# Optimization experiments

Hardware: AMD Instinct MI355X
Metric: run time of the kernel (lower is better)

## Reference

```python
import jax, jax.numpy as jnp
import numpy as np

B, N, C = 64, 197, 768
H = 12
D = C // H
SCALE = D ** -0.5
TAU = 5.0
THRESHOLD = 0.6
NEG_INF = float('-inf')


def setup_inputs() -> dict:
    key = jax.random.key(0)
    ks = jax.random.split(key, 10)
    def gumbel(k, shape):
        # -log(Exponential) == standard Gumbel noise, matches torch exponential_().log()
        e = jax.random.exponential(k, shape, dtype=jnp.float32)
        return -jnp.log(e + 1e-10)
    s = 0.02
    return {
        'x': jax.random.normal(ks[0], (B, N, C), dtype=jnp.float32),
        'g1': gumbel(ks[1], (B, N - 1, 1)),
        'g2': gumbel(ks[2], (B, N - 1, 1)),
        'Wq': jax.random.normal(ks[3], (C, C), dtype=jnp.float32) * s,
        'Wk': jax.random.normal(ks[4], (C, C), dtype=jnp.float32) * s,
        'Wv': jax.random.normal(ks[5], (C, C), dtype=jnp.float32) * s,
        'Wp': jax.random.normal(ks[6], (C, C), dtype=jnp.float32) * s,
        'bp': jnp.zeros((C,), dtype=jnp.float32),
        'Wm': jax.random.normal(ks[7], (1, C), dtype=jnp.float32) * s,
        'bm': jnp.zeros((1,), dtype=jnp.float32),
    }


def reference(x, g1, g2, Wq, Wk, Wv, Wp, bp, Wm, bm):
    b, n, c = x.shape
    # QKV projections (qkv_bias=False), reshape to (B, H, N, D)
    q = (x @ Wq.T).reshape(b, n, H, D).transpose(0, 2, 1, 3)
    k = (x @ Wk.T).reshape(b, n, H, D).transpose(0, 2, 1, 3)
    v = (x @ Wv.T).reshape(b, n, H, D).transpose(0, 2, 1, 3)

    attn_pre = jnp.einsum('bhnd,bhmd->bhnm', q, k) * SCALE  # (B,H,N,N)

    # SimpleTokenSelect: gumbel-sigmoid gating on non-CLS tokens (training=True, hard=True)
    logits = x[:, 1:] @ Wm.T + bm                       # (B, N-1, 1)
    y_soft = jax.nn.sigmoid((logits + g1 - g2) / TAU)
    y_hard = (y_soft > THRESHOLD).astype(y_soft.dtype)
    ts = y_hard - jax.lax.stop_gradient(y_soft) + y_soft  # straight-through
    ts = jnp.concatenate([jnp.ones((b, 1, 1), dtype=ts.dtype), ts], axis=1)[..., 0]  # (B, N)

    # attention policy = outer product of token gates, detached (ada_token_detach_attn)
    policy = jax.lax.stop_gradient(jnp.einsum('bn,bm->bnm', ts, ts))[:, None]  # (B,1,N,N)

    # pre-softmax masking: zero gated scores, -inf off-diagonal entries of gated rows
    eye = jnp.eye(n, dtype=attn_pre.dtype)
    neg_mask = jnp.where(1.0 - policy - eye > 0, NEG_INF, 0.0)
    attn = jax.nn.softmax(attn_pre * policy + neg_mask, axis=-1)

    out = jnp.einsum('bhnm,bhmd->bhnd', attn, v)        # (B,H,N,D)
    out = out.transpose(0, 2, 1, 3).reshape(b, n, c)
    out = out @ Wp.T + bp                                # proj (dropout p=0)
    return out
```

## Files before the change

kernel.cpp:

```cpp
#include <hip/hip_runtime.h>
#include <hip/hip_bf16.h>
#include <cstdint>

typedef unsigned short u16;
typedef __attribute__((ext_vector_type(8))) short bf16x8;
typedef __attribute__((ext_vector_type(4))) float f32x4;

#define NB 64
#define NN 197
#define NC 768
#define NH 12
#define ND 64
#define NM (NB*NN)
#define CAP 96
#define NT 24
#define ASZ ((size_t)NM*NC)
#define WSZ ((size_t)NC*NC)
#define SELSZ ((size_t)NB*CAP*NC)

#define WAITVM(N) asm volatile("s_waitcnt vmcnt(" #N ")" ::: "memory")
#define SBAR() __builtin_amdgcn_s_barrier()
#define SCHEDB() __builtin_amdgcn_sched_barrier(0)

__device__ __forceinline__ u16 f2bf(float f) {
  uint32_t u = __float_as_uint(f);
  u += 0x7fffu + ((u >> 16) & 1u);
  return (u16)(u >> 16);
}

__device__ __forceinline__ void gl_lds16(const u16* g, u16* l) {
  __builtin_amdgcn_global_load_lds(
      (const __attribute__((address_space(1))) void*)g,
      (__attribute__((address_space(3))) void*)l, 16, 0, 0);
}

__device__ __forceinline__ int self_compact(const float* __restrict__ ts, int b,
                                            int* sidx, unsigned long long* bmask) {
  int t = threadIdx.x, lane = t & 63, wave = t >> 6;
  bool sel = (t < NN) && (ts[b * NN + t] > 0.5f);
  unsigned long long m = __ballot(sel);
  if (lane == 0) bmask[wave] = m;
  for (int i = t; i < CAP; i += 256) sidx[i] = 0;
  __syncthreads();
  int before = 0, total = 0;
  #pragma unroll
  for (int w = 0; w < 4; ++w) {
    int c = __popcll(bmask[w]);
    total += c;
    if (w < wave) before += c;
  }
  int within = __popcll(bmask[wave] & ((lane == 0) ? 0ull : (~0ull >> (64 - lane))));
  int pos = before + within;
  int cntc = total < CAP ? total : CAP;
  if (sel && pos < CAP) sidx[pos] = t;
  __syncthreads();
  return cntc;
}

#define GATEB 3152
#define WBLK 576
#define TRBLK 144
__global__ __launch_bounds__(256) void k1_prep(const float* __restrict__ x,
    const float* __restrict__ g1, const float* __restrict__ g2,
    const float* __restrict__ Wm, const float* __restrict__ bm,
    const float* __restrict__ wq, const float* __restrict__ wk,
    const float* __restrict__ wv, const float* __restrict__ wp,
    u16* __restrict__ xb, u16* __restrict__ wqb, u16* __restrict__ wkb,
    u16* __restrict__ wvb, u16* __restrict__ wpb, u16* __restrict__ wvt,
    float* __restrict__ ts) {
  __shared__ u16 T[64][72];
  int bid = blockIdx.x, tid = threadIdx.x;

  if (bid < GATEB) {
    int wave = tid >> 6, lane = tid & 63;
    int wid = bid * 4 + wave;
    int b = wid / NN, n = wid % NN;
    const float* xr = x + (size_t)wid * NC;
    u16* xbr = xb + (size_t)wid * NC;
    double acc = 0.0;
    #pragma unroll
    for (int i = 0; i < 3; ++i) {
      float4 f = *(const float4*)(xr + lane * 4 + 256 * i);
      float4 w = *(const float4*)(Wm + lane * 4 + 256 * i);
      acc += (double)f.x * w.x + (double)f.y * w.y
           + (double)f.z * w.z + (double)f.w * w.w;
      ushort4 o;
      o.x = f2bf(f.x); o.y = f2bf(f.y); o.z = f2bf(f.z); o.w = f2bf(f.w);
      *(ushort4*)(xbr + lane * 4 + 256 * i) = o;
    }
    #pragma unroll
    for (int off = 32; off; off >>= 1) acc += __shfl_down(acc, off);
    float o = 1.0f;
    if (n != 0) {
      double z = (acc + (double)bm[0] + (double)g1[b*(NN-1) + n - 1]
                                      - (double)g2[b*(NN-1) + n - 1]) / 5.0;
      o = (z > 0.4054651081081643820) ? 1.0f : 0.0f;
    }
    if (lane == 0) ts[wid] = o;
    return;
  }
  bid -= GATEB;
  if (bid < 4*WBLK) {
    int seg = bid / WBLK;
    int i = (bid - seg * WBLK) * 256 + tid;
    const float* src; u16* dst;
    if (seg == 0)      { src = wq; dst = wqb; }
    else if (seg == 1) { src = wk; dst = wkb; }
    else if (seg == 2) { src = wv; dst = wvb; }
    else               { src = wp; dst = wpb; }
    float4 f = ((const float4*)src)[i];
    ushort4 o;
    o.x = f2bf(f.x); o.y = f2bf(f.y); o.z = f2bf(f.z); o.w = f2bf(f.w);
    ((ushort4*)dst)[i] = o;
    return;
  }
  bid -= 4*WBLK;
  {
    int bx = bid % 12, by = bid / 12;
    int j0 = by * 64, k0 = bx * 64;
    #pragma unroll
    for (int g = 0; g < 4; ++g) {
      int r = g * 16 + (tid >> 4);
      int c4 = (tid & 15) * 4;
      float4 f = *(const float4*)(wv + (size_t)(j0 + r) * NC + k0 + c4);
      T[c4 + 0][r] = f2bf(f.x);
      T[c4 + 1][r] = f2bf(f.y);
      T[c4 + 2][r] = f2bf(f.z);
      T[c4 + 3][r] = f2bf(f.w);
    }
    __syncthreads();
    #pragma unroll
    for (int g = 0; g < 4; ++g) {
      int r = g * 16 + (tid >> 4);
      int c4 = (tid & 15) * 4;
      ushort4 o = *(ushort4*)&T[r][c4];
      *(ushort4*)(wvt + (size_t)(k0 + r) * NC + j0 + c4) = o;
    }
  }
}

__global__ __launch_bounds__(256) void k2_wvp_qkv(const u16* __restrict__ xb,
    const u16* __restrict__ wq3, const u16* __restrict__ wpb,
    const u16* __restrict__ wvt, u16* __restrict__ wvpb,
    u16* __restrict__ sel3, const float* __restrict__ ts) {
  alignas(16) __shared__ u16 SA[3][128][32];
  alignas(16) __shared__ u16 SB[3][128][32];
  __shared__ int sidx[CAP];
  __shared__ unsigned long long bmask[4];
  int bid = blockIdx.x;
  int tid = threadIdx.x, lane = tid & 63, wave = tid >> 6;
  int lr = lane & 15, lg = lane >> 4, lk = lg * 8;

  if (bid < 36) {
    int m0 = (bid / 6) * 128, n0 = (bid % 6) * 128;
    int wr = (wave >> 1) * 64, wc = (wave & 1) * 64;
    f32x4 acc[4][4];
    #pragma unroll
    for (int i = 0; i < 4; ++i)
      #pragma unroll
      for (int j = 0; j < 4; ++j) acc[i][j] = (f32x4){0.f,0.f,0.f,0.f};
    auto stage = [&](int buf, int kt) {
      int k0 = kt * 32;
      #pragma unroll
      for (int i = 0; i < 2; ++i) {
        int c = wave * 2 + i;
        int id = c * 64 + lane;
        int row = id >> 2, col8 = (id & 3) * 8;
        gl_lds16(wpb + (size_t)(m0 + row) * NC + k0 + col8, &SA[buf][0][0] + c * 512);
        gl_lds16(wvt + (size_t)(n0 + row) * NC + k0 + col8, &SB[buf][0][0] + c * 512);
      }
    };
    auto comp = [&](int buf) {
      bf16x8 af[4], bfr[4];
      #pragma unroll
      for (int f = 0; f < 4; ++f) {
        af[f]  = *(const bf16x8*)(&SA[buf][wr + f*16 + lr][lk]);
        bfr[f] = *(const bf16x8*)(&SB[buf][wc + f*16 + lr][lk]);
      }
      #pragma unroll
      for (int i = 0; i < 4; ++i)
        #pragma unroll
        for (int j = 0; j < 4; ++j)
          acc[i][j] = __builtin_amdgcn_mfma_f32_16x16x32_bf16(af[i], bfr[j], acc[i][j], 0, 0, 0);
    };
    stage(0, 0); stage(1, 1);
    int cb = 0;
    for (int t = 0; t < NT; ++t) {
      if (t + 2 < NT) {
        int sb = cb + 2; if (sb > 2) sb -= 3;
        stage(sb, t + 2);
        WAITVM(8);
      } else if (t + 1 < NT) { WAITVM(4); }
      else { WAITVM(0); }
      SBAR(); SCHEDB();
      comp(cb);
      SBAR();
      cb = (cb == 2) ? 0 : cb + 1;
    }
    #pragma unroll
    for (int i = 0; i < 4; ++i)
      #pragma unroll
      for (int j = 0; j < 4; ++j)
        #pragma unroll
        for (int r = 0; r < 4; ++r)
          wvpb[(size_t)(m0 + wr + i*16 + 4*lg + r) * NC + n0 + wc + j*16 + lr] =
              f2bf(acc[i][j][r]);
    return;
  }

  int t0 = bid - 36;
  int gb = t0 / 18, r18 = t0 % 18;
  int y = r18 / 3, z = r18 % 3;
  int b = gb / 3, rc = gb % 3;
  int cntb = self_compact(ts, b, sidx, bmask);
  if (rc * 32 >= cntb) return;
  const u16* W = wq3 + (size_t)z * WSZ;
  u16* o = sel3 + (size_t)z * SELSZ;
  int n0 = y * 128;

  int chA = wave * 64 + lane;
  int tokA = sidx[rc * 32 + (chA >> 2)];
  const u16* baseA = xb + (size_t)(b * NN + tokA) * NC + (chA & 3) * 8;
  int chB0 = wave * 64 + lane, chB1 = 256 + wave * 64 + lane;
  const u16* baseB0 = W + (size_t)(n0 + (chB0 >> 2)) * NC + (chB0 & 3) * 8;
  const u16* baseB1 = W + (size_t)(n0 + (chB1 >> 2)) * NC + (chB1 & 3) * 8;

  int wc = wave * 32;
  bool hasA = (wave < 2);
  f32x4 acc[2][2];
  #pragma unroll
  for (int i = 0; i < 2; ++i)
    #pragma unroll
    for (int j = 0; j < 2; ++j) acc[i][j] = (f32x4){0.f,0.f,0.f,0.f};

  auto stageS = [&](int buf, int kt) {
    int k0 = kt * 32;
    if (hasA) gl_lds16(baseA + k0, &SA[buf][0][0] + (size_t)(wave * 64) * 8);
    gl_lds16(baseB0 + k0, &SB[buf][0][0] + (size_t)(wave * 64) * 8);
    gl_lds16(baseB1 + k0, &SB[buf][0][0] + (size_t)(256 + wave * 64) * 8);
  };
  auto compS = [&](int buf) {
    bf16x8 af[2], bfr[2];
    #pragma unroll
    for (int f = 0; f < 2; ++f) {
      af[f]  = *(const bf16x8*)(&SA[buf][f*16 + lr][lk]);
      bfr[f] = *(const bf16x8*)(&SB[buf][wc + f*16 + lr][lk]);
    }
    #pragma unroll
    for (int i = 0; i < 2; ++i)
      #pragma unroll
      for (int j = 0; j < 2; ++j)
        acc[i][j] = __builtin_amdgcn_mfma_f32_16x16x32_bf16(af[i], bfr[j], acc[i][j], 0, 0, 0);
  };
  stageS(0, 0); stageS(1, 1);
  int cb = 0;
  for (int tt = 0; tt < NT; ++tt) {
    if (tt + 2 < NT) {
      int sb = cb + 2; if (sb > 2) sb -= 3;
      stageS(sb, tt + 2);
      if (hasA) { WAITVM(6); } else { WAITVM(4); }
    } else if (tt + 1 < NT) {
      if (hasA) { WAITVM(3); } else { WAITVM(2); }
    } else { WAITVM(0); }
    SBAR(); SCHEDB();
    compS(cb);
    SBAR();
    cb = (cb == 2) ? 0 : cb + 1;
  }

  #pragma unroll
  for (int i = 0; i < 2; ++i)
    #pragma unroll
    for (int j = 0; j < 2; ++j)
      #pragma unroll
      for (int r = 0; r < 4; ++r) {
        int rsel = rc*32 + i*16 + 4*lg + r;
        if (rsel < cntb)
          o[(size_t)(b * CAP + rsel) * NC + n0 + wc + j*16 + lr] = f2bf(acc[i][j][r]);
      }
}

__global__ __launch_bounds__(256) void attn_sel(const u16* __restrict__ qsel,
    const u16* __restrict__ ksel, const u16* __restrict__ vsel,
    u16* __restrict__ zsel, const float* __restrict__ ts) {
  alignas(16) __shared__ u16 Vt[64][232];
  __shared__ unsigned long long bmask[4];
  int bh = blockIdx.x;
  int b = bh / NH, h = bh % NH;
  int tid = threadIdx.x, lane = tid & 63, wave = tid >> 6;
  int lr = lane & 15, lg = lane >> 4;
  const size_t qbase = (size_t)b * CAP * NC + (size_t)h * ND;

  bool selt = (tid < NN) && (ts[b * NN + tid] > 0.5f);
  unsigned long long m = __ballot(selt);
  if (lane == 0) bmask[wave] = m;
  __syncthreads();
  int cntb = 0;
  #pragma unroll
  for (int w = 0; w < 4; ++w) cntb += __popcll(bmask[w]);
  if (cntb > CAP) cntb = CAP;

  for (int id = tid; id < cntb * 8; id += 256) {
    int i = id >> 3, c8 = (id & 7) * 8;
    int4 val = *(const int4*)(vsel + qbase + (size_t)i * NC + c8);
    u16 tmp[8];
    *(int4*)tmp = val;
    #pragma unroll
    for (int e = 0; e < 8; ++e) Vt[c8 + e][i] = tmp[e];
  }
  for (int id = tid; id < 64 * 32; id += 256)
    Vt[id >> 5][cntb + (id & 31)] = 0;
  __syncthreads();

  int nchunk = (cntb + 15) >> 4;
  int mtmax  = nchunk;
  int mcmax  = (cntb + 31) >> 5;
  int idx0 = (((lane & 15) | ((lane & 16) << 1))) << 2;
  int idx1 = idx0 + 64;

  for (int qc = wave; qc < nchunk; qc += 4) {
    const u16* qp = qsel + qbase + (size_t)(qc * 16 + lr) * NC + lg * 8;
    bf16x8 qf0 = *(const bf16x8*)(qp);
    bf16x8 qf1 = *(const bf16x8*)(qp + 32);

    f32x4 s[6];
    #pragma unroll
    for (int mt = 0; mt < 6; ++mt) s[mt] = (f32x4){0.f,0.f,0.f,0.f};
    #pragma unroll
    for (int mt = 0; mt < 6; ++mt) {
      if (mt < mtmax) {
        const u16* kp = ksel + qbase + (size_t)(mt * 16 + lr) * NC + lg * 8;
        bf16x8 kf0 = *(const bf16x8*)(kp);
        bf16x8 kf1 = *(const bf16x8*)(kp + 32);
        f32x4 a = (f32x4){0.f,0.f,0.f,0.f};
        a = __builtin_amdgcn_mfma_f32_16x16x32_bf16(kf0, qf0, a, 0, 0, 0);
        a = __builtin_amdgcn_mfma_f32_16x16x32_bf16(kf1, qf1, a, 0, 0, 0);
        s[mt] = a;
      }
    }

    float mx = -3e38f;
    #pragma unroll
    for (int mt = 0; mt < 6; ++mt)
      #pragma unroll
      for (int jj = 0; jj < 4; ++jj) {
        int mm = mt*16 + 4*lg + jj;
        float val = (mm < cntb) ? s[mt][jj] * 0.125f : -1e30f;
        s[mt][jj] = val;
        mx = fmaxf(mx, val);
      }
    mx = fmaxf(mx, __shfl_xor(mx, 16));
    mx = fmaxf(mx, __shfl_xor(mx, 32));
    float sum = 0.f;
    #pragma unroll
    for (int mt = 0; mt < 6; ++mt)
      #pragma unroll
      for (int jj = 0; jj < 4; ++jj) {
        float pv = __expf(s[mt][jj] - mx);
        s[mt][jj] = pv;
        sum += pv;
      }
    sum += __shfl_xor(sum, 16);
    sum += __shfl_xor(sum, 32);
    float inv = 1.0f / sum;

    uint32_t u[6][2];
    #pragma unroll
    for (int mt = 0; mt < 6; ++mt) {
      u[mt][0] = ((uint32_t)f2bf(s[mt][1]*inv) << 16) | f2bf(s[mt][0]*inv);
      u[mt][1] = ((uint32_t)f2bf(s[mt][3]*inv) << 16) | f2bf(s[mt][2]*inv);
    }

    f32x4 oacc[4];
    #pragma unroll
    for (int dt = 0; dt < 4; ++dt) oacc[dt] = (f32x4){0.f,0.f,0.f,0.f};
    #pragma unroll
    for (int mc = 0; mc < 3; ++mc) {
      if (mc < mcmax) {
        uint32_t a0 = (uint32_t)__builtin_amdgcn_ds_bpermute(idx0, (int)u[2*mc][0]);
        uint32_t b0 = (uint32_t)__builtin_amdgcn_ds_bpermute(idx0, (int)u[2*mc+1][0]);
        uint32_t a1 = (uint32_t)__builtin_amdgcn_ds_bpermute(idx0, (int)u[2*mc][1]);
        uint32_t b1 = (uint32_t)__builtin_amdgcn_ds_bpermute(idx0, (int)u[2*mc+1][1]);
        uint32_t a2 = (uint32_t)__builtin_amdgcn_ds_bpermute(idx1, (int)u[2*mc][0]);
        uint32_t b2 = (uint32_t)__builtin_amdgcn_ds_bpermute(idx1, (int)u[2*mc+1][0]);
        uint32_t a3 = (uint32_t)__builtin_amdgcn_ds_bpermute(idx1, (int)u[2*mc][1]);
        uint32_t b3 = (uint32_t)__builtin_amdgcn_ds_bpermute(idx1, (int)u[2*mc+1][1]);
        bool hi = (lg >= 2);
        union { uint32_t w[4]; bf16x8 v; } pu;
        pu.w[0] = hi ? b0 : a0;
        pu.w[1] = hi ? b1 : a1;
        pu.w[2] = hi ? b2 : a2;
        pu.w[3] = hi ? b3 : a3;
        bf16x8 pa = pu.v;
        #pragma unroll
        for (int dt = 0; dt < 4; ++dt) {
          bf16x8 vf = *(const bf16x8*)(&Vt[dt*16 + lr][mc*32 + lg*8]);
          oacc[dt] = __builtin_amdgcn_mfma_f32_16x16x32_bf16(pa, vf, oacc[dt], 0, 0, 0);
        }
      }
    }

    #pragma unroll
    for (int r = 0; r < 4; ++r) {
      int nloc = qc*16 + 4*lg + r;
      if (nloc < cntb) {
        u16* op = zsel + qbase + (size_t)nloc * NC + lr;
        #pragma unroll
        for (int dt = 0; dt < 4; ++dt)
          op[dt*16] = f2bf(oacc[dt][r]);
      }
    }
  }
}

#define DBLK 594
#define PBLK 1152
__global__ __launch_bounds__(256) void k4_out(const u16* __restrict__ xb,
    const u16* __restrict__ wvpb, const u16* __restrict__ zsel,
    const u16* __restrict__ wpb, const float* __restrict__ ts,
    const float* __restrict__ bp, float* __restrict__ out) {
  alignas(16) __shared__ u16 SA[3][128][32];
  alignas(16) __shared__ u16 SB[3][128][32];
  __shared__ int sidx[CAP];
  __shared__ unsigned long long bmask[4];
  int bid = blockIdx.x;
  int tid = threadIdx.x, lane = tid & 63, wave = tid >> 6;
  int lr = lane & 15, lg = lane >> 4, lk = lg * 8;

  if (bid < DBLK) {
    int orig = bid;
    int xcd = orig & 7, loc = orig >> 3;
    int wgid = (xcd < 2 ? xcd * 75 : 150 + (xcd - 2) * 74) + loc;
    int m0 = (wgid / 6) * 128, n0 = (wgid % 6) * 128;
    int wr = (wave >> 1) * 64, wc = (wave & 1) * 64;
    f32x4 acc[4][4];
    #pragma unroll
    for (int i = 0; i < 4; ++i)
      #pragma unroll
      for (int j = 0; j < 4; ++j) acc[i][j] = (f32x4){0.f,0.f,0.f,0.f};
    auto stage = [&](int buf, int kt) {
      int k0 = kt * 32;
      #pragma unroll
      for (int i = 0; i < 2; ++i) {
        int c = wave * 2 + i;
        int id = c * 64 + lane;
        int row = id >> 2, col8 = (id & 3) * 8;
        gl_lds16(xb + (size_t)(m0 + row) * NC + k0 + col8, &SA[buf][0][0] + c * 512);
        gl_lds16(wvpb + (size_t)(n0 + row) * NC + k0 + col8, &SB[buf][0][0] + c * 512);
      }
    };
    auto comp = [&](int buf) {
      bf16x8 af[4], bfr[4];
      #pragma unroll
      for (int f = 0; f < 4; ++f) {
        af[f]  = *(const bf16x8*)(&SA[buf][wr + f*16 + lr][lk]);
        bfr[f] = *(const bf16x8*)(&SB[buf][wc + f*16 + lr][lk]);
      }
      #pragma unroll
      for (int i = 0; i < 4; ++i)
        #pragma unroll
        for (int j = 0; j < 4; ++j)
          acc[i][j] = __builtin_amdgcn_mfma_f32_16x16x32_bf16(af[i], bfr[j], acc[i][j], 0, 0, 0);
    };
    stage(0, 0); stage(1, 1);
    int cb = 0;
    for (int t = 0; t < NT; ++t) {
      if (t + 2 < NT) {
        int sb = cb + 2; if (sb > 2) sb -= 3;
        stage(sb, t + 2);
        WAITVM(8);
      } else if (t + 1 < NT) { WAITVM(4); }
      else { WAITVM(0); }
      SBAR(); SCHEDB();
      comp(cb);
      SBAR();
      cb = (cb == 2) ? 0 : cb + 1;
    }
    #pragma unroll
    for (int i = 0; i < 4; ++i) {
      int rbase = m0 + wr + i*16 + 4*lg;
      #pragma unroll
      for (int j = 0; j < 4; ++j) {
        int col = n0 + wc + j*16 + lr;
        #pragma unroll
        for (int r = 0; r < 4; ++r) {
          int row = rbase + r;
          if (row < NM && ts[row] < 0.5f)
            out[(size_t)row * NC + col] = acc[i][j][r] + bp[col];
        }
      }
    }
    return;
  }

  int t = bid - DBLK;
  int gb = t / 6, y = t % 6;
  int b = gb / 3, rc = gb % 3;
  int cntb = self_compact(ts, b, sidx, bmask);
  if (rc * 32 >= cntb) return;
  int n0 = y * 128;

  int chA = wave * 64 + lane;
  const u16* baseA = zsel + (size_t)(b * CAP + rc * 32 + (chA >> 2)) * NC + (chA & 3) * 8;
  int chB0 = wave * 64 + lane, chB1 = 256 + wave * 64 + lane;
  const u16* baseB0 = wpb + (size_t)(n0 + (chB0 >> 2)) * NC + (chB0 & 3) * 8;
  const u16* baseB1 = wpb + (size_t)(n0 + (chB1 >> 2)) * NC + (chB1 & 3) * 8;

  int wc = wave * 32;
  f32x4 acc[2][2];
  #pragma unroll
  for (int i = 0; i < 2; ++i)
    #pragma unroll
    for (int j = 0; j < 2; ++j) acc[i][j] = (f32x4){0.f,0.f,0.f,0.f};

  auto stageS = [&](int buf, int k0) {
    if (wave < 2) gl_lds16(baseA + k0, &SA[buf][0][0] + (size_t)(wave * 64) * 8);
    gl_lds16(baseB0 + k0, &SB[buf][0][0] + (size_t)(wave * 64) * 8);
    gl_lds16(baseB1 + k0, &SB[buf][0][0] + (size_t)(256 + wave * 64) * 8);
  };
  auto compS = [&](int buf) {
    bf16x8 af[2], bfr[2];
    #pragma unroll
    for (int f = 0; f < 2; ++f) {
      af[f]  = *(const bf16x8*)(&SA[buf][f*16 + lr][lk]);
      bfr[f] = *(const bf16x8*)(&SB[buf][wc + f*16 + lr][lk]);
    }
    #pragma unroll
    for (int i = 0; i < 2; ++i)
      #pragma unroll
      for (int j = 0; j < 2; ++j)
        acc[i][j] = __builtin_amdgcn_mfma_f32_16x16x32_bf16(af[i], bfr[j], acc[i][j], 0, 0, 0);
  };
  stageS(0, 0);
  __syncthreads();
  int cur = 0;
  for (int tt = 0; tt < NT - 1; ++tt) {
    stageS(cur ^ 1, (tt + 1) * 32);
    compS(cur);
    __syncthreads();
    cur ^= 1;
  }
  compS(cur);

  #pragma unroll
  for (int i = 0; i < 2; ++i)
    #pragma unroll
    for (int j = 0; j < 2; ++j)
      #pragma unroll
      for (int r = 0; r < 4; ++r) {
        int rsel = rc*32 + i*16 + 4*lg + r;
        if (rsel < cntb) {
          int tok = sidx[rsel];
          int col = n0 + wc + j*16 + lr;
          out[(size_t)(b * NN + tok) * NC + col] = acc[i][j][r] + bp[col];
        }
      }
}

extern "C" void kernel_launch(void* const* d_in, const int* in_sizes, int n_in,
                              void* d_out, int out_size, void* d_ws, size_t ws_size,
                              hipStream_t stream) {
  const float* x  = (const float*)d_in[0];
  const float* g1 = (const float*)d_in[1];
  const float* g2 = (const float*)d_in[2];
  const float* Wq = (const float*)d_in[3];
  const float* Wk = (const float*)d_in[4];
  const float* Wv = (const float*)d_in[5];
  const float* Wp = (const float*)d_in[6];
  const float* bp = (const float*)d_in[7];
  const float* Wm = (const float*)d_in[8];
  const float* bm = (const float*)d_in[9];
  float* out = (float*)d_out;

  const size_t act_sz = ASZ * 2;
  const size_t w_sz   = WSZ * 2;
  const size_t sel_sz = SELSZ * 2;
  size_t need = act_sz + 4*sel_sz + 6*w_sz + (size_t)NM*4 + 256;
  if (ws_size < need) return;

  char* p = (char*)d_ws;
  u16* xb   = (u16*)p; p += act_sz;
  u16* qsel = (u16*)p; p += sel_sz;
  u16* ksel = (u16*)p; p += sel_sz;
  u16* vsel = (u16*)p; p += sel_sz;
  u16* zsel = (u16*)p; p += sel_sz;
  u16* wqb  = (u16*)p; p += w_sz;
  u16* wkb  = (u16*)p; p += w_sz;
  u16* wvb  = (u16*)p; p += w_sz;
  u16* wpb  = (u16*)p; p += w_sz;
  u16* wvtb = (u16*)p; p += w_sz;
  u16* wvpb = (u16*)p; p += w_sz;
  float* ts = (float*)p;
  (void)wkb; (void)wvb;

  k1_prep<<<dim3(GATEB + 4*WBLK + TRBLK), 256, 0, stream>>>(
      x, g1, g2, Wm, bm, Wq, Wk, Wv, Wp,
      xb, wqb, wkb, wvb, wpb, wvtb, ts);

  k2_wvp_qkv<<<dim3(36 + NB*3*18), 256, 0, stream>>>(
      xb, wqb, wpb, wvtb, wvpb, qsel, ts);

  attn_sel<<<dim3(NB*NH), 256, 0, stream>>>(qsel, ksel, vsel, zsel, ts);

  k4_out<<<dim3(DBLK + PBLK), 256, 0, stream>>>(
      xb, wvpb, zsel, wpb, ts, bp, out);
}
```

Baseline: 108.1 us.

## Shrink dense out-GEMM tile to 128x64, single-buffer LDS, share union LDS

Halves the N-tile of the dense V·Wp GEMM path from 128 to 64 columns, doubling its block count and remapping the XCD-aware block-to-tile assignment. The triple-buffered async pipeline is replaced with a simple single-buffer load/sync/compute/sync loop. LDS is merged into one union buffer shared by the dense and the sparse path. The aim is lower per-block LDS and register use, giving more blocks for occupancy and load balance, at the cost of losing load/compute overlap and re-reading A tiles twice.

```diff
diff --git a/kernel.cpp b/kernel.cpp
--- a/kernel.cpp
+++ b/kernel.cpp
@@ -413,14 +413,13 @@
   }
 }
 
-#define DBLK 594
+#define DBLK 1188
 #define PBLK 1152
 __global__ __launch_bounds__(256) void k4_out(const u16* __restrict__ xb,
     const u16* __restrict__ wvpb, const u16* __restrict__ zsel,
     const u16* __restrict__ wpb, const float* __restrict__ ts,
     const float* __restrict__ bp, float* __restrict__ out) {
-  alignas(16) __shared__ u16 SA[3][128][32];
-  alignas(16) __shared__ u16 SB[3][128][32];
+  alignas(16) __shared__ u16 LDSU[10496];
   __shared__ int sidx[CAP];
   __shared__ unsigned long long bmask[4];
   int bid = blockIdx.x;
@@ -428,59 +427,50 @@
   int lr = lane & 15, lg = lane >> 4, lk = lg * 8;
 
   if (bid < DBLK) {
-    int orig = bid;
-    int xcd = orig & 7, loc = orig >> 3;
-    int wgid = (xcd < 2 ? xcd * 75 : 150 + (xcd - 2) * 74) + loc;
-    int m0 = (wgid / 6) * 128, n0 = (wgid % 6) * 128;
-    int wr = (wave >> 1) * 64, wc = (wave & 1) * 64;
-    f32x4 acc[4][4];
+    u16 (*As)[32] = reinterpret_cast<u16(*)[32]>(&LDSU[0]);
+    u16 (*Bs)[32] = reinterpret_cast<u16(*)[32]>(&LDSU[4096]);
+    int xcd = bid & 7, loc = bid >> 3;
+    int wgid = (xcd < 4 ? xcd * 149 : 596 + (xcd - 4) * 148) + loc;
+    int m0 = (wgid / 12) * 128, n0 = (wgid % 12) * 64;
+    int wr = (wave >> 1) * 64, wc = (wave & 1) * 32;
+    int idA0 = wave * 64 + lane;
+    int idA1 = (4 + wave) * 64 + lane;
+    int idB  = wave * 64 + lane;
+    const u16* srcA0 = xb + (size_t)(m0 + (idA0 >> 2)) * NC + (idA0 & 3) * 8;
+    const u16* srcA1 = xb + (size_t)(m0 + (idA1 >> 2)) * NC + (idA1 & 3) * 8;
+    const u16* srcB  = wvpb + (size_t)(n0 + (idB >> 2)) * NC + (idB & 3) * 8;
+    u16* dA0 = &As[0][0] + (size_t)wave * 512;
+    u16* dA1 = &As[0][0] + (size_t)(4 + wave) * 512;
+    u16* dB  = &Bs[0][0] + (size_t)wave * 512;
+
+    f32x4 acc[4][2];
     #pragma unroll
     for (int i = 0; i < 4; ++i)
       #pragma unroll
-      for (int j = 0; j < 4; ++j) acc[i][j] = (f32x4){0.f,0.f,0.f,0.f};
-    auto stage = [&](int buf, int kt) {
-      int k0 = kt * 32;
-      #pragma unroll
-      for (int i = 0; i < 2; ++i) {
-        int c = wave * 2 + i;
-        int id = c * 64 + lane;
-        int row = id >> 2, col8 = (id & 3) * 8;
-        gl_lds16(xb + (size_t)(m0 + row) * NC + k0 + col8, &SA[buf][0][0] + c * 512);
-        gl_lds16(wvpb + (size_t)(n0 + row) * NC + k0 + col8, &SB[buf][0][0] + c * 512);
-      }
-    };
-    auto comp = [&](int buf) {
-      bf16x8 af[4], bfr[4];
-      #pragma unroll
-      for (int f = 0; f < 4; ++f) {
-        af[f]  = *(const bf16x8*)(&SA[buf][wr + f*16 + lr][lk]);
-        bfr[f] = *(const bf16x8*)(&SB[buf][wc + f*16 + lr][lk]);
-      }
+      for (int j = 0; j < 2; ++j) acc[i][j] = (f32x4){0.f,0.f,0.f,0.f};
+
+    for (int k0 = 0; k0 < NC; k0 += 32) {
+      gl_lds16(srcA0 + k0, dA0);
+      gl_lds16(srcA1 + k0, dA1);
+      gl_lds16(srcB + k0, dB);
+      __syncthreads();
+      bf16x8 af[4], bfr[2];
+      #pragma unroll
+      for (int f = 0; f < 4; ++f) af[f] = *(const bf16x8*)(&As[wr + f*16 + lr][lk]);
+      #pragma unroll
+      for (int f = 0; f < 2; ++f) bfr[f] = *(const bf16x8*)(&Bs[wc + f*16 + lr][lk]);
       #pragma unroll
       for (int i = 0; i < 4; ++i)
         #pragma unroll
-        for (int j = 0; j < 4; ++j)
+        for (int j = 0; j < 2; ++j)
           acc[i][j] = __builtin_amdgcn_mfma_f32_16x16x32_bf16(af[i], bfr[j], acc[i][j], 0, 0, 0);
-    };
-    stage(0, 0); stage(1, 1);
-    int cb = 0;
-    for (int t = 0; t < NT; ++t) {
-      if (t + 2 < NT) {
-        int sb = cb + 2; if (sb > 2) sb -= 3;
-        stage(sb, t + 2);
-        WAITVM(8);
-      } else if (t + 1 < NT) { WAITVM(4); }
-      else { WAITVM(0); }
-      SBAR(); SCHEDB();
-      comp(cb);
-      SBAR();
-      cb = (cb == 2) ? 0 : cb + 1;
+      __syncthreads();
     }
     #pragma unroll
     for (int i = 0; i < 4; ++i) {
       int rbase = m0 + wr + i*16 + 4*lg;
       #pragma unroll
-      for (int j = 0; j < 4; ++j) {
+      for (int j = 0; j < 2; ++j) {
         int col = n0 + wc + j*16 + lr;
         #pragma unroll
         for (int r = 0; r < 4; ++r) {
@@ -493,6 +483,8 @@
     return;
   }
 
+  u16 (*PA)[32][32]  = reinterpret_cast<u16(*)[32][32]>(&LDSU[0]);
+  u16 (*PB)[128][32] = reinterpret_cast<u16(*)[128][32]>(&LDSU[2048]);
   int t = bid - DBLK;
   int gb = t / 6, y = t % 6;
   int b = gb / 3, rc = gb % 3;
@@ -514,16 +506,16 @@
     for (int j = 0; j < 2; ++j) acc[i][j] = (f32x4){0.f,0.f,0.f,0.f};
 
   auto stageS = [&](int buf, int k0) {
-    if (wave < 2) gl_lds16(baseA + k0, &SA[buf][0][0] + (size_t)(wave * 64) * 8);
-    gl_lds16(baseB0 + k0, &SB[buf][0][0] + (size_t)(wave * 64) * 8);
-    gl_lds16(baseB1 + k0, &SB[buf][0][0] + (size_t)(256 + wave * 64) * 8);
+    if (wave < 2) gl_lds16(baseA + k0, &PA[buf][0][0] + (size_t)(wave * 64) * 8);
+    gl_lds16(baseB0 + k0, &PB[buf][0][0] + (size_t)(wave * 64) * 8);
+    gl_lds16(baseB1 + k0, &PB[buf][0][0] + (size_t)(256 + wave * 64) * 8);
   };
   auto compS = [&](int buf) {
     bf16x8 af[2], bfr[2];
     #pragma unroll
     for (int f = 0; f < 2; ++f) {
-      af[f]  = *(const bf16x8*)(&SA[buf][f*16 + lr][lk]);
-      bfr[f] = *(const bf16x8*)(&SB[buf][wc + f*16 + lr][lk]);
+      af[f]  = *(const bf16x8*)(&PA[buf][f*16 + lr][lk]);
+      bfr[f] = *(const bf16x8*)(&PB[buf][wc + f*16 + lr][lk]);
     }
     #pragma unroll
     for (int i = 0; i < 2; ++i)
```

After: 108.4 us. About the same (+0.3%).

## Globally compact selected tokens into packed rows for full-size 128x128 GEMM tiles

Applied to the files above, without the earlier changes.

Adds a single-block compaction kernel that builds a global index of gated tokens across all batches with per-batch offsets. The selected-row QKV and output-projection GEMMs then run as dense 128x128 MFMA tiles over the packed rows, replacing per-batch 32-row tiles that wasted work and recomputed the compaction in every block. In exchange, the new selected and dense k4 GEMM loops lose the triple-buffered pipeline and become single-buffered with two barriers per k-step. The serial single-block compaction launch adds latency on the critical path.

```diff
diff --git a/kernel.cpp b/kernel.cpp
--- a/kernel.cpp
+++ b/kernel.cpp
@@ -14,9 +14,11 @@
 #define NM (NB*NN)
 #define CAP 96
 #define NT 24
+#define SELR 6144
+#define MSELT 48
 #define ASZ ((size_t)NM*NC)
 #define WSZ ((size_t)NC*NC)
-#define SELSZ ((size_t)NB*CAP*NC)
+#define SELSZ2 ((size_t)SELR*NC)
 
 #define WAITVM(N) asm volatile("s_waitcnt vmcnt(" #N ")" ::: "memory")
 #define SBAR() __builtin_amdgcn_s_barrier()
@@ -32,29 +34,6 @@
   __builtin_amdgcn_global_load_lds(
       (const __attribute__((address_space(1))) void*)g,
       (__attribute__((address_space(3))) void*)l, 16, 0, 0);
-}
-
-__device__ __forceinline__ int self_compact(const float* __restrict__ ts, int b,
-                                            int* sidx, unsigned long long* bmask) {
-  int t = threadIdx.x, lane = t & 63, wave = t >> 6;
-  bool sel = (t < NN) && (ts[b * NN + t] > 0.5f);
-  unsigned long long m = __ballot(sel);
-  if (lane == 0) bmask[wave] = m;
-  for (int i = t; i < CAP; i += 256) sidx[i] = 0;
-  __syncthreads();
-  int before = 0, total = 0;
-  #pragma unroll
-  for (int w = 0; w < 4; ++w) {
-    int c = __popcll(bmask[w]);
-    total += c;
-    if (w < wave) before += c;
-  }
-  int within = __popcll(bmask[wave] & ((lane == 0) ? 0ull : (~0ull >> (64 - lane))));
-  int pos = before + within;
-  int cntc = total < CAP ? total : CAP;
-  if (sel && pos < CAP) sidx[pos] = t;
-  __syncthreads();
-  return cntc;
 }
 
 #define GATEB 3152
@@ -139,166 +118,181 @@
   }
 }
 
+__global__ __launch_bounds__(256) void ck_compact(const float* __restrict__ ts,
+    int* __restrict__ cnt, int* __restrict__ boff, int* __restrict__ gidx) {
+  __shared__ unsigned long long bm[4];
+  __shared__ int runoff;
+  int tid = threadIdx.x, lane = tid & 63, wave = tid >> 6;
+  if (tid == 0) runoff = 0;
+  __syncthreads();
+  for (int b = 0; b < NB; ++b) {
+    bool sel = (tid < NN) && (ts[b * NN + tid] > 0.5f);
+    unsigned long long m = __ballot(sel);
+    if (lane == 0) bm[wave] = m;
+    __syncthreads();
+    int before = 0, total = 0;
+    #pragma unroll
+    for (int w = 0; w < 4; ++w) {
+      int c = __popcll(bm[w]);
+      total += c;
+      if (w < wave) before += c;
+    }
+    int within = __popcll(bm[wave] & ((lane == 0) ? 0ull : (~0ull >> (64 - lane))));
+    int pos = before + within;
+    int cc = total < CAP ? total : CAP;
+    int base = runoff;
+    if (sel && pos < CAP) gidx[base + pos] = b * NN + tid;
+    __syncthreads();
+    if (tid == 0) { cnt[b] = cc; boff[b] = base; runoff = base + cc; }
+    __syncthreads();
+  }
+  int tot = runoff;
+  if (tid == 0) boff[NB] = tot;
+  for (int i = tot + tid; i < SELR; i += 256) gidx[i] = 0;
+}
+
 __global__ __launch_bounds__(256) void k2_wvp_qkv(const u16* __restrict__ xb,
     const u16* __restrict__ wq3, const u16* __restrict__ wpb,
     const u16* __restrict__ wvt, u16* __restrict__ wvpb,
-    u16* __restrict__ sel3, const float* __restrict__ ts) {
+    u16* __restrict__ sel3, const int* __restrict__ boff,
+    const int* __restrict__ gidx) {
   alignas(16) __shared__ u16 SA[3][128][32];
   alignas(16) __shared__ u16 SB[3][128][32];
-  __shared__ int sidx[CAP];
-  __shared__ unsigned long long bmask[4];
   int bid = blockIdx.x;
   int tid = threadIdx.x, lane = tid & 63, wave = tid >> 6;
   int lr = lane & 15, lg = lane >> 4, lk = lg * 8;
 
-  if (bid < 36) {
-    int m0 = (bid / 6) * 128, n0 = (bid % 6) * 128;
+  if (bid < MSELT * 18) {
+    int mt = bid / 18, r18 = bid % 18;
+    int z = r18 / 6, y = r18 % 6;
+    int total = boff[NB];
+    int m0 = mt * 128;
+    if (m0 >= total) return;
+    const u16* W = wq3 + (size_t)z * WSZ;
+    u16* o = sel3 + (size_t)z * SELSZ2;
+    int n0 = y * 128;
     int wr = (wave >> 1) * 64, wc = (wave & 1) * 64;
+
+    int id0 = (wave*2 + 0) * 64 + lane, id1 = (wave*2 + 1) * 64 + lane;
+    const u16* baseA0 = xb + (size_t)gidx[m0 + (id0 >> 2)] * NC + (id0 & 3) * 8;
+    const u16* baseA1 = xb + (size_t)gidx[m0 + (id1 >> 2)] * NC + (id1 & 3) * 8;
+    const u16* baseB0 = W + (size_t)(n0 + (id0 >> 2)) * NC + (id0 & 3) * 8;
+    const u16* baseB1 = W + (size_t)(n0 + (id1 >> 2)) * NC + (id1 & 3) * 8;
+    u16* dA0 = &SA[0][0][0] + (size_t)(wave*2 + 0) * 512;
+    u16* dA1 = &SA[0][0][0] + (size_t)(wave*2 + 1) * 512;
+    u16* dB0 = &SB[0][0][0] + (size_t)(wave*2 + 0) * 512;
+    u16* dB1 = &SB[0][0][0] + (size_t)(wave*2 + 1) * 512;
+
     f32x4 acc[4][4];
     #pragma unroll
     for (int i = 0; i < 4; ++i)
       #pragma unroll
       for (int j = 0; j < 4; ++j) acc[i][j] = (f32x4){0.f,0.f,0.f,0.f};
-    auto stage = [&](int buf, int kt) {
-      int k0 = kt * 32;
-      #pragma unroll
-      for (int i = 0; i < 2; ++i) {
-        int c = wave * 2 + i;
-        int id = c * 64 + lane;
-        int row = id >> 2, col8 = (id & 3) * 8;
-        gl_lds16(wpb + (size_t)(m0 + row) * NC + k0 + col8, &SA[buf][0][0] + c * 512);
-        gl_lds16(wvt + (size_t)(n0 + row) * NC + k0 + col8, &SB[buf][0][0] + c * 512);
-      }
-    };
-    auto comp = [&](int buf) {
+
+    for (int k0 = 0; k0 < NC; k0 += 32) {
+      gl_lds16(baseA0 + k0, dA0);
+      gl_lds16(baseA1 + k0, dA1);
+      gl_lds16(baseB0 + k0, dB0);
+      gl_lds16(baseB1 + k0, dB1);
+      __syncthreads();
       bf16x8 af[4], bfr[4];
       #pragma unroll
       for (int f = 0; f < 4; ++f) {
-        af[f]  = *(const bf16x8*)(&SA[buf][wr + f*16 + lr][lk]);
-        bfr[f] = *(const bf16x8*)(&SB[buf][wc + f*16 + lr][lk]);
+        af[f]  = *(const bf16x8*)(&SA[0][wr + f*16 + lr][lk]);
+        bfr[f] = *(const bf16x8*)(&SB[0][wc + f*16 + lr][lk]);
       }
       #pragma unroll
       for (int i = 0; i < 4; ++i)
         #pragma unroll
         for (int j = 0; j < 4; ++j)
           acc[i][j] = __builtin_amdgcn_mfma_f32_16x16x32_bf16(af[i], bfr[j], acc[i][j], 0, 0, 0);
-    };
-    stage(0, 0); stage(1, 1);
-    int cb = 0;
-    for (int t = 0; t < NT; ++t) {
-      if (t + 2 < NT) {
-        int sb = cb + 2; if (sb > 2) sb -= 3;
-        stage(sb, t + 2);
-        WAITVM(8);
-      } else if (t + 1 < NT) { WAITVM(4); }
-      else { WAITVM(0); }
-      SBAR(); SCHEDB();
-      comp(cb);
-      SBAR();
-      cb = (cb == 2) ? 0 : cb + 1;
+      __syncthreads();
+    }
+    #pragma unroll
+    for (int i = 0; i < 4; ++i) {
+      int rbase = m0 + wr + i*16 + 4*lg;
+      #pragma unroll
+      for (int j = 0; j < 4; ++j) {
+        int col = n0 + wc + j*16 + lr;
+        #pragma unroll
+        for (int r = 0; r < 4; ++r) {
+          int row = rbase + r;
+          if (row < total)
+            o[(size_t)row * NC + col] = f2bf(acc[i][j][r]);
+        }
+      }
+    }
+    return;
+  }
+
+  int wb = bid - MSELT * 18;
+  int m0 = (wb / 6) * 128, n0 = (wb % 6) * 128;
+  int wr = (wave >> 1) * 64, wc = (wave & 1) * 64;
+  f32x4 acc[4][4];
+  #pragma unroll
+  for (int i = 0; i < 4; ++i)
+    #pragma unroll
+    for (int j = 0; j < 4; ++j) acc[i][j] = (f32x4){0.f,0.f,0.f,0.f};
+  auto stage = [&](int buf, int kt) {
+    int k0 = kt * 32;
+    #pragma unroll
+    for (int i = 0; i < 2; ++i) {
+      int c = wave * 2 + i;
+      int id = c * 64 + lane;
+      int row = id >> 2, col8 = (id & 3) * 8;
+      gl_lds16(wpb + (size_t)(m0 + row) * NC + k0 + col8, &SA[buf][0][0] + c * 512);
+      gl_lds16(wvt + (size_t)(n0 + row) * NC + k0 + col8, &SB[buf][0][0] + c * 512);
+    }
+  };
+  auto comp = [&](int buf) {
+    bf16x8 af[4], bfr[4];
+    #pragma unroll
+    for (int f = 0; f < 4; ++f) {
+      af[f]  = *(const bf16x8*)(&SA[buf][wr + f*16 + lr][lk]);
+      bfr[f] = *(const bf16x8*)(&SB[buf][wc + f*16 + lr][lk]);
     }
     #pragma unroll
     for (int i = 0; i < 4; ++i)
       #pragma unroll
       for (int j = 0; j < 4; ++j)
-        #pragma unroll
-        for (int r = 0; r < 4; ++r)
-          wvpb[(size_t)(m0 + wr + i*16 + 4*lg + r) * NC + n0 + wc + j*16 + lr] =
-              f2bf(acc[i][j][r]);
-    return;
-  }
-
-  int t0 = bid - 36;
-  int gb = t0 / 18, r18 = t0 % 18;
-  int y = r18 / 3, z = r18 % 3;
-  int b = gb / 3, rc = gb % 3;
-  int cntb = self_compact(ts, b, sidx, bmask);
-  if (rc * 32 >= cntb) return;
-  const u16* W = wq3 + (size_t)z * WSZ;
-  u16* o = sel3 + (size_t)z * SELSZ;
-  int n0 = y * 128;
-
-  int chA = wave * 64 + lane;
-  int tokA = sidx[rc * 32 + (chA >> 2)];
-  const u16* baseA = xb + (size_t)(b * NN + tokA) * NC + (chA & 3) * 8;
-  int chB0 = wave * 64 + lane, chB1 = 256 + wave * 64 + lane;
-  const u16* baseB0 = W + (size_t)(n0 + (chB0 >> 2)) * NC + (chB0 & 3) * 8;
-  const u16* baseB1 = W + (size_t)(n0 + (chB1 >> 2)) * NC + (chB1 & 3) * 8;
-
-  int wc = wave * 32;
-  bool hasA = (wave < 2);
-  f32x4 acc[2][2];
-  #pragma unroll
-  for (int i = 0; i < 2; ++i)
-    #pragma unroll
-    for (int j = 0; j < 2; ++j) acc[i][j] = (f32x4){0.f,0.f,0.f,0.f};
-
-  auto stageS = [&](int buf, int kt) {
-    int k0 = kt * 32;
-    if (hasA) gl_lds16(baseA + k0, &SA[buf][0][0] + (size_t)(wave * 64) * 8);
-    gl_lds16(baseB0 + k0, &SB[buf][0][0] + (size_t)(wave * 64) * 8);
-    gl_lds16(baseB1 + k0, &SB[buf][0][0] + (size_t)(256 + wave * 64) * 8);
-  };
-  auto compS = [&](int buf) {
-    bf16x8 af[2], bfr[2];
-    #pragma unroll
-    for (int f = 0; f < 2; ++f) {
-      af[f]  = *(const bf16x8*)(&SA[buf][f*16 + lr][lk]);
-      bfr[f] = *(const bf16x8*)(&SB[buf][wc + f*16 + lr][lk]);
-    }
-    #pragma unroll
-    for (int i = 0; i < 2; ++i)
-      #pragma unroll
-      for (int j = 0; j < 2; ++j)
         acc[i][j] = __builtin_amdgcn_mfma_f32_16x16x32_bf16(af[i], bfr[j], acc[i][j], 0, 0, 0);
   };
-  stageS(0, 0); stageS(1, 1);
+  stage(0, 0); stage(1, 1);
   int cb = 0;
-  for (int tt = 0; tt < NT; ++tt) {
-    if (tt + 2 < NT) {
+  for (int t = 0; t < NT; ++t) {
+    if (t + 2 < NT) {
       int sb = cb + 2; if (sb > 2) sb -= 3;
-      stageS(sb, tt + 2);
-      if (hasA) { WAITVM(6); } else { WAITVM(4); }
-    } else if (tt + 1 < NT) {
-      if (hasA) { WAITVM(3); } else { WAITVM(2); }
-    } else { WAITVM(0); }
+      stage(sb, t + 2);
+      WAITVM(8);
+    } else if (t + 1 < NT) { WAITVM(4); }
+    else { WAITVM(0); }
     SBAR(); SCHEDB();
-    compS(cb);
+    comp(cb);
     SBAR();
     cb = (cb == 2) ? 0 : cb + 1;
   }
-
   #pragma unroll
-  for (int i = 0; i < 2; ++i)
-    #pragma unroll
-    for (int j = 0; j < 2; ++j)
-      #pragma unroll
-      for (int r = 0; r < 4; ++r) {
-        int rsel = rc*32 + i*16 + 4*lg + r;
-        if (rsel < cntb)
-          o[(size_t)(b * CAP + rsel) * NC + n0 + wc + j*16 + lr] = f2bf(acc[i][j][r]);
-      }
+  for (int i = 0; i < 4; ++i)
+    #pragma unroll
+    for (int j = 0; j < 4; ++j)
+      #pragma unroll
+      for (int r = 0; r < 4; ++r)
+        wvpb[(size_t)(m0 + wr + i*16 + 4*lg + r) * NC + n0 + wc + j*16 + lr] =
+            f2bf(acc[i][j][r]);
 }
 
 __global__ __launch_bounds__(256) void attn_sel(const u16* __restrict__ qsel,
     const u16* __restrict__ ksel, const u16* __restrict__ vsel,
-    u16* __restrict__ zsel, const float* __restrict__ ts) {
+    u16* __restrict__ zsel, const int* __restrict__ cnt,
+    const int* __restrict__ boff) {
   alignas(16) __shared__ u16 Vt[64][232];
-  __shared__ unsigned long long bmask[4];
   int bh = blockIdx.x;
   int b = bh / NH, h = bh % NH;
+  int cntb = cnt[b];
+  int boffb = boff[b];
   int tid = threadIdx.x, lane = tid & 63, wave = tid >> 6;
   int lr = lane & 15, lg = lane >> 4;
-  const size_t qbase = (size_t)b * CAP * NC + (size_t)h * ND;
-
-  bool selt = (tid < NN) && (ts[b * NN + tid] > 0.5f);
-  unsigned long long m = __ballot(selt);
-  if (lane == 0) bmask[wave] = m;
-  __syncthreads();
-  int cntb = 0;
-  #pragma unroll
-  for (int w = 0; w < 4; ++w) cntb += __popcll(bmask[w]);
-  if (cntb > CAP) cntb = CAP;
+  const size_t qbase = (size_t)boffb * NC + (size_t)h * ND;
 
   for (int id = tid; id < cntb * 8; id += 256) {
     int i = id >> 3, c8 = (id & 7) * 8;
@@ -414,68 +408,75 @@
 }
 
 #define DBLK 594
-#define PBLK 1152
+#define PJBLK (MSELT*6)
 __global__ __launch_bounds__(256) void k4_out(const u16* __restrict__ xb,
     const u16* __restrict__ wvpb, const u16* __restrict__ zsel,
     const u16* __restrict__ wpb, const float* __restrict__ ts,
-    const float* __restrict__ bp, float* __restrict__ out) {
-  alignas(16) __shared__ u16 SA[3][128][32];
-  alignas(16) __shared__ u16 SB[3][128][32];
-  __shared__ int sidx[CAP];
-  __shared__ unsigned long long bmask[4];
+    const float* __restrict__ bp, float* __restrict__ out,
+    const int* __restrict__ boff, const int* __restrict__ gidx) {
+  alignas(16) __shared__ u16 SA[128][32];
+  alignas(16) __shared__ u16 SB[128][32];
   int bid = blockIdx.x;
   int tid = threadIdx.x, lane = tid & 63, wave = tid >> 6;
   int lr = lane & 15, lg = lane >> 4, lk = lg * 8;
-
-  if (bid < DBLK) {
-    int orig = bid;
-    int xcd = orig & 7, loc = orig >> 3;
+  int wr = (wave >> 1) * 64, wc = (wave & 1) * 64;
+
+  const u16* Abase; const u16* Bbase;
+  int m0, n0, total = 0;
+  bool dense = (bid < DBLK);
+  if (dense) {
+    int xcd = bid & 7, loc = bid >> 3;
     int wgid = (xcd < 2 ? xcd * 75 : 150 + (xcd - 2) * 74) + loc;
-    int m0 = (wgid / 6) * 128, n0 = (wgid % 6) * 128;
-    int wr = (wave >> 1) * 64, wc = (wave & 1) * 64;
-    f32x4 acc[4][4];
+    m0 = (wgid / 6) * 128;
+    n0 = (wgid % 6) * 128;
+    Abase = xb; Bbase = wvpb;
+  } else {
+    int pid = bid - DBLK;
+    int mt = pid / 6, y = pid % 6;
+    total = boff[NB];
+    m0 = mt * 128;
+    if (m0 >= total) return;
+    n0 = y * 128;
+    Abase = zsel; Bbase = wpb;
+  }
+
+  int id0 = (wave*2 + 0) * 64 + lane, id1 = (wave*2 + 1) * 64 + lane;
+  const u16* baseA0 = Abase + (size_t)(m0 + (id0 >> 2)) * NC + (id0 & 3) * 8;
+  const u16* baseA1 = Abase + (size_t)(m0 + (id1 >> 2)) * NC + (id1 & 3) * 8;
+  const u16* baseB0 = Bbase + (size_t)(n0 + (id0 >> 2)) * NC + (id0 & 3) * 8;
+  const u16* baseB1 = Bbase + (size_t)(n0 + (id1 >> 2)) * NC + (id1 & 3) * 8;
+  u16* dA0 = &SA[0][0] + (size_t)(wave*2 + 0) * 512;
+  u16* dA1 = &SA[0][0] + (size_t)(wave*2 + 1) * 512;
+  u16* dB0 = &SB[0][0] + (size_t)(wave*2 + 0) * 512;
+  u16* dB1 = &SB[0][0] + (size_t)(wave*2 + 1) * 512;
+
+  f32x4 acc[4][4];
+  #pragma unroll
+  for (int i = 0; i < 4; ++i)
+    #pragma unroll
+    for (int j = 0; j < 4; ++j) acc[i][j] = (f32x4){0.f,0.f,0.f,0.f};
+
+  for (int k0 = 0; k0 < NC; k0 += 32) {
+    gl_lds16(baseA0 + k0, dA0);
+    gl_lds16(baseA1 + k0, dA1);
+    gl_lds16(baseB0 + k0, dB0);
+    gl_lds16(baseB1 + k0, dB1);
+    __syncthreads();
+    bf16x8 af[4], bfr[4];
+    #pragma unroll
+    for (int f = 0; f < 4; ++f) {
+      af[f]  = *(const bf16x8*)(&SA[wr + f*16 + lr][lk]);
+      bfr[f] = *(const bf16x8*)(&SB[wc + f*16 + lr][lk]);
+    }
     #pragma unroll
     for (int i = 0; i < 4; ++i)
       #pragma unroll
-      for (int j = 0; j < 4; ++j) acc[i][j] = (f32x4){0.f,0.f,0.f,0.f};
-    auto stage = [&](int buf, int kt) {
-      int k0 = kt * 32;
-      #pragma unroll
-      for (int i = 0; i < 2; ++i) {
-        int c = wave * 2 + i;
-        int id = c * 64 + lane;
-        int row = id >> 2, col8 = (id & 3) * 8;
-        gl_lds16(xb + (size_t)(m0 + row) * NC + k0 + col8, &SA[buf][0][0] + c * 512);
-        gl_lds16(wvpb + (size_t)(n0 + row) * NC + k0 + col8, &SB[buf][0][0] + c * 512);
-      }
-    };
-    auto comp = [&](int buf) {
-      bf16x8 af[4], bfr[4];
-      #pragma unroll
-      for (int f = 0; f < 4; ++f) {
-        af[f]  = *(const bf16x8*)(&SA[buf][wr + f*16 + lr][lk]);
-        bfr[f] = *(const bf16x8*)(&SB[buf][wc + f*16 + lr][lk]);
-      }
-      #pragma unroll
-      for (int i = 0; i < 4; ++i)
-        #pragma unroll
-        for (int j = 0; j < 4; ++j)
-          acc[i][j] = __builtin_amdgcn_mfma_f32_16x16x32_bf16(af[i], bfr[j], acc[i][j], 0, 0, 0);
-    };
-    stage(0, 0); stage(1, 1);
-    int cb = 0;
-    for (int t = 0; t < NT; ++t) {
-      if (t + 2 < NT) {
-        int sb = cb + 2; if (sb > 2) sb -= 3;
-        stage(sb, t + 2);
-        WAITVM(8);
-      } else if (t + 1 < NT) { WAITVM(4); }
-      else { WAITVM(0); }
-      SBAR(); SCHEDB();
-      comp(cb);
-      SBAR();
-      cb = (cb == 2) ? 0 : cb + 1;
-    }
+      for (int j = 0; j < 4; ++j)
+        acc[i][j] = __builtin_amdgcn_mfma_f32_16x16x32_bf16(af[i], bfr[j], acc[i][j], 0, 0, 0);
+    __syncthreads();
+  }
+
+  if (dense) {
     #pragma unroll
     for (int i = 0; i < 4; ++i) {
       int rbase = m0 + wr + i*16 + 4*lg;
@@ -490,71 +491,24 @@
         }
       }
     }
-    return;
-  }
-
-  int t = bid - DBLK;
-  int gb = t / 6, y = t % 6;
-  int b = gb / 3, rc = gb % 3;
-  int cntb = self_compact(ts, b, sidx, bmask);
-  if (rc * 32 >= cntb) return;
-  int n0 = y * 128;
-
-  int chA = wave * 64 + lane;
-  const u16* baseA = zsel + (size_t)(b * CAP + rc * 32 + (chA >> 2)) * NC + (chA & 3) * 8;
-  int chB0 = wave * 64 + lane, chB1 = 256 + wave * 64 + lane;
-  const u16* baseB0 = wpb + (size_t)(n0 + (chB0 >> 2)) * NC + (chB0 & 3) * 8;
-  const u16* baseB1 = wpb + (size_t)(n0 + (chB1 >> 2)) * NC + (chB1 & 3) * 8;
-
-  int wc = wave * 32;
-  f32x4 acc[2][2];
-  #pragma unroll
-  for (int i = 0; i < 2; ++i)
-    #pragma unroll
-    for (int j = 0; j < 2; ++j) acc[i][j] = (f32x4){0.f,0.f,0.f,0.f};
-
-  auto stageS = [&](int buf, int k0) {
-    if (wave < 2) gl_lds16(baseA + k0, &SA[buf][0][0] + (size_t)(wave * 64) * 8);
-    gl_lds16(baseB0 + k0, &SB[buf][0][0] + (size_t)(wave * 64) * 8);
-    gl_lds16(baseB1 + k0, &SB[buf][0][0] + (size_t)(256 + wave * 64) * 8);
-  };
-  auto compS = [&](int buf) {
-    bf16x8 af[2], bfr[2];
-    #pragma unroll
-    for (int f = 0; f < 2; ++f) {
-      af[f]  = *(const bf16x8*)(&SA[buf][f*16 + lr][lk]);
-      bfr[f] = *(const bf16x8*)(&SB[buf][wc + f*16 + lr][lk]);
-    }
-    #pragma unroll
-    for (int i = 0; i < 2; ++i)
-      #pragma unroll
-      for (int j = 0; j < 2; ++j)
-        acc[i][j] = __builtin_amdgcn_mfma_f32_16x16x32_bf16(af[i], bfr[j], acc[i][j], 0, 0, 0);
-  };
-  stageS(0, 0);
-  __syncthreads();
-  int cur = 0;
-  for (int tt = 0; tt < NT - 1; ++tt) {
-    stageS(cur ^ 1, (tt + 1) * 32);
-    compS(cur);
-    __syncthreads();
-    cur ^= 1;
-  }
-  compS(cur);
-
-  #pragma unroll
-  for (int i = 0; i < 2; ++i)
-    #pragma unroll
-    for (int j = 0; j < 2; ++j)
-      #pragma unroll
-      for (int r = 0; r < 4; ++r) {
-        int rsel = rc*32 + i*16 + 4*lg + r;
-        if (rsel < cntb) {
-          int tok = sidx[rsel];
-          int col = n0 + wc + j*16 + lr;
-          out[(size_t)(b * NN + tok) * NC + col] = acc[i][j][r] + bp[col];
+  } else {
+    #pragma unroll
+    for (int i = 0; i < 4; ++i) {
+      int rbase = m0 + wr + i*16 + 4*lg;
+      #pragma unroll
+      for (int j = 0; j < 4; ++j) {
+        int col = n0 + wc + j*16 + lr;
+        #pragma unroll
+        for (int r = 0; r < 4; ++r) {
+          int row = rbase + r;
+          if (row < total) {
+            int grow = gidx[row];
+            out[(size_t)grow * NC + col] = acc[i][j][r] + bp[col];
+          }
         }
       }
+    }
+  }
 }
 
 extern "C" void kernel_launch(void* const* d_in, const int* in_sizes, int n_in,
@@ -574,8 +528,9 @@
 
   const size_t act_sz = ASZ * 2;
   const size_t w_sz   = WSZ * 2;
-  const size_t sel_sz = SELSZ * 2;
-  size_t need = act_sz + 4*sel_sz + 6*w_sz + (size_t)NM*4 + 256;
+  const size_t sel_sz = SELSZ2 * 2;
+  size_t need = act_sz + 4*sel_sz + 6*w_sz + (size_t)NM*4
+              + (size_t)(NB+1)*4 + (size_t)NB*4 + (size_t)SELR*4 + 256;
   if (ws_size < need) return;
 
   char* p = (char*)d_ws;
@@ -590,18 +545,23 @@
   u16* wpb  = (u16*)p; p += w_sz;
   u16* wvtb = (u16*)p; p += w_sz;
   u16* wvpb = (u16*)p; p += w_sz;
-  float* ts = (float*)p;
+  float* ts = (float*)p; p += (size_t)NM*4;
+  int* cnt  = (int*)p;  p += (size_t)NB*4;
+  int* boff = (int*)p;  p += (size_t)(NB+1)*4;
+  int* gidx = (int*)p;
   (void)wkb; (void)wvb;
 
   k1_prep<<<dim3(GATEB + 4*WBLK + TRBLK), 256, 0, stream>>>(
       x, g1, g2, Wm, bm, Wq, Wk, Wv, Wp,
       xb, wqb, wkb, wvb, wpb, wvtb, ts);
 
-  k2_wvp_qkv<<<dim3(36 + NB*3*18), 256, 0, stream>>>(
-      xb, wqb, wpb, wvtb, wvpb, qsel, ts);
-
-  attn_sel<<<dim3(NB*NH), 256, 0, stream>>>(qsel, ksel, vsel, zsel, ts);
-
-  k4_out<<<dim3(DBLK + PBLK), 256, 0, stream>>>(
-      xb, wvpb, zsel, wpb, ts, bp, out);
-}
+  ck_compact<<<dim3(1), 256, 0, stream>>>(ts, cnt, boff, gidx);
+
+  k2_wvp_qkv<<<dim3(MSELT*18 + 36), 256, 0, stream>>>(
+      xb, wqb, wpb, wvtb, wvpb, qsel, boff, gidx);
+
+  attn_sel<<<dim3(NB*NH), 256, 0, stream>>>(qsel, ksel, vsel, zsel, cnt, boff);
+
+  k4_out<<<dim3(DBLK + PJBLK), 256, 0, stream>>>(
+      xb, wvpb, zsel, wpb, ts, bp, out, boff, gidx);
+}
```

After: 118.1 us. +9.3%, slower.
